# Kernel tuning notes

Hardware: AMD Instinct MI355X
Metric: run time of the kernel (lower is better)

Reference implementation:

```python
import jax, jax.numpy as jnp
import numpy as np

N, A, C = 65536, 512, 1000


def setup_inputs() -> dict:
    key = jax.random.key(0)
    k1, k2, k3, k4, k5 = jax.random.split(key, 5)
    return {
        "features": jax.random.normal(k1, (N, A), dtype=jnp.float32),
        "labels": jax.random.randint(k2, (N,), 0, C),
        "count": jax.random.uniform(k3, (C,), dtype=jnp.float32) * 100.0,
        "mean": jax.random.normal(k4, (C, A), dtype=jnp.float32),
        "cov": jax.random.uniform(k5, (C, A), dtype=jnp.float32),
    }


def reference(features, labels, count, mean, cov):
    # Per-class counts and feature sums via segment reduction (math identical to
    # the torch onehot-expand NxCxA construction, but O(N*A) instead of O(N*C*A)).
    c = count.shape[0]
    ones = jnp.ones((features.shape[0],), dtype=features.dtype)
    n_c = jax.ops.segment_sum(ones, labels, num_segments=c)            # [C]
    sums = jax.ops.segment_sum(features, labels, num_segments=c)      # [C, A]
    amt = jnp.where(n_c == 0, 1.0, n_c)                                # Amount_CxA (zeros -> 1)
    ave = sums / amt[:, None]                                          # ave_CxA
    diff = features - ave[labels]                                      # onehot*(x - ave) per row
    var = jax.ops.segment_sum(diff * diff, labels, num_segments=c) / amt[:, None]
    # EMA blend weight; torch sets NaN (0/0) entries to 0.
    denom = n_c + count
    w = jnp.where(denom == 0, 0.0, n_c / jnp.where(denom == 0, 1.0, denom))[:, None]  # [C,1]
    cov_new = cov * (1.0 - w) + var * w + w * (1.0 - w) * (mean - ave) ** 2
    mean_new = mean * (1.0 - w) + ave * w
    count_new = count + n_c
    return cov_new, mean_new, count_new
```

## Files before the change

### kernel.cpp

```cpp
#include <hip/hip_runtime.h>

constexpr int N_ROWS  = 65536;
constexpr int N_FEAT  = 512;
constexpr int N_FEAT2 = N_FEAT / 2;
constexpr int N_CLS   = 1000;


__global__ __launch_bounds__(1024) void hist_scan_kernel(
    const int* __restrict__ labels, int* __restrict__ offs, int* __restrict__ cursor)
{
    __shared__ int bins[1024];
    __shared__ int tmp[1024];
    const int t = threadIdx.x;
    bins[t] = 0;
    __syncthreads();

    const int4* __restrict__ l4 = (const int4*)labels;
    #pragma unroll 4
    for (int i = t; i < N_ROWS / 4; i += 1024) {
        int4 v = l4[i];
        atomicAdd(&bins[v.x], 1); atomicAdd(&bins[v.y], 1);
        atomicAdd(&bins[v.z], 1); atomicAdd(&bins[v.w], 1);
    }
    __syncthreads();

    const int v = bins[t];
    tmp[t] = v;
    __syncthreads();
    for (int d = 1; d < 1024; d <<= 1) {
        int x = (t >= d) ? tmp[t - d] : 0;
        __syncthreads();
        tmp[t] += x;
        __syncthreads();
    }
    const int excl = tmp[t] - v;
    offs[t] = excl;
    cursor[t] = excl;
    if (t == 0) offs[1024] = N_ROWS;
}

__global__ __launch_bounds__(256) void scatter_kernel(
    const int* __restrict__ labels, int* __restrict__ cursor, int* __restrict__ perm)
{
    const int i = blockIdx.x * blockDim.x + threadIdx.x;
    const int4 v = ((const int4*)labels)[i];
    const int r = i * 4;
    perm[atomicAdd(&cursor[v.x], 1)] = r + 0;
    perm[atomicAdd(&cursor[v.y], 1)] = r + 1;
    perm[atomicAdd(&cursor[v.z], 1)] = r + 2;
    perm[atomicAdd(&cursor[v.w], 1)] = r + 3;
}

__global__ __launch_bounds__(256) void estimator_main(
    const float* __restrict__ features,
    const float* __restrict__ count,
    const float* __restrict__ mean,
    const float* __restrict__ cov,
    const int* __restrict__ offs,
    const int* __restrict__ perm,
    float* __restrict__ out)
{
    const int c = blockIdx.x;
    const int t = threadIdx.x;
    const int start = offs[c];
    const int n = offs[c + 1] - start;

    __shared__ int sh[256];
    const float2* __restrict__ f2 = (const float2*)features;

    float sx = 0.f, sy = 0.f, qx = 0.f, qy = 0.f;

    for (int base = 0; base < n; base += 256) {
        const int chunk = min(256, n - base);
        __syncthreads();
        if (t < chunk) sh[t] = perm[start + base + t];
        __syncthreads();
        int j = 0;
        for (; j + 8 <= chunk; j += 8) {
            const int r0 = sh[j+0], r1 = sh[j+1], r2 = sh[j+2], r3 = sh[j+3];
            const int r4 = sh[j+4], r5 = sh[j+5], r6 = sh[j+6], r7 = sh[j+7];
            const float2 v0 = f2[(size_t)r0 * N_FEAT2 + t];
            const float2 v1 = f2[(size_t)r1 * N_FEAT2 + t];
            const float2 v2 = f2[(size_t)r2 * N_FEAT2 + t];
            const float2 v3 = f2[(size_t)r3 * N_FEAT2 + t];
            const float2 v4 = f2[(size_t)r4 * N_FEAT2 + t];
            const float2 v5 = f2[(size_t)r5 * N_FEAT2 + t];
            const float2 v6 = f2[(size_t)r6 * N_FEAT2 + t];
            const float2 v7 = f2[(size_t)r7 * N_FEAT2 + t];
            sx += v0.x; sy += v0.y; qx += v0.x*v0.x; qy += v0.y*v0.y;
            sx += v1.x; sy += v1.y; qx += v1.x*v1.x; qy += v1.y*v1.y;
            sx += v2.x; sy += v2.y; qx += v2.x*v2.x; qy += v2.y*v2.y;
            sx += v3.x; sy += v3.y; qx += v3.x*v3.x; qy += v3.y*v3.y;
            sx += v4.x; sy += v4.y; qx += v4.x*v4.x; qy += v4.y*v4.y;
            sx += v5.x; sy += v5.y; qx += v5.x*v5.x; qy += v5.y*v5.y;
            sx += v6.x; sy += v6.y; qx += v6.x*v6.x; qy += v6.y*v6.y;
            sx += v7.x; sy += v7.y; qx += v7.x*v7.x; qy += v7.y*v7.y;
        }
        for (; j < chunk; ++j) {
            const float2 v = f2[(size_t)sh[j] * N_FEAT2 + t];
            sx += v.x; sy += v.y; qx += v.x*v.x; qy += v.y*v.y;
        }
    }

    const float fn  = (float)n;
    const float amt = (n > 0) ? fn : 1.0f;
    const float inv = 1.0f / amt;
    const float avx = sx * inv, avy = sy * inv;
    const float vrx = qx * inv - avx * avx;
    const float vry = qy * inv - avy * avy;

    const float cnt   = count[c];
    const float denom = fn + cnt;
    const float w     = (denom == 0.f) ? 0.f : fn / denom;
    const float omw   = 1.0f - w;

    const float2 mv = ((const float2*)mean)[c * N_FEAT2 + t];
    const float2 cv = ((const float2*)cov)[c * N_FEAT2 + t];
    const float dx = mv.x - avx, dy = mv.y - avy;

    float2 covn, meann;
    covn.x  = cv.x * omw + vrx * w + w * omw * dx * dx;
    covn.y  = cv.y * omw + vry * w + w * omw * dy * dy;
    meann.x = mv.x * omw + avx * w;
    meann.y = mv.y * omw + avy * w;

    ((float2*)out)[c * N_FEAT2 + t] = covn;
    ((float2*)(out + N_CLS * N_FEAT))[c * N_FEAT2 + t] = meann;
    if (t == 0) out[2 * N_CLS * N_FEAT + c] = cnt + fn;
}

extern "C" void kernel_launch(void* const* d_in, const int* in_sizes, int n_in,
                              void* d_out, int out_size, void* d_ws, size_t ws_size,
                              hipStream_t stream) {
    const float* features = (const float*)d_in[0];
    const int*   labels   = (const int*)d_in[1];
    const float* count    = (const float*)d_in[2];
    const float* mean     = (const float*)d_in[3];
    const float* cov      = (const float*)d_in[4];
    float* out = (float*)d_out;

    char* ws = (char*)d_ws;
    int* offs   = (int*)(ws + 0);
    int* cursor = (int*)(ws + 8192);
    int* perm   = (int*)(ws + 12288);

    hist_scan_kernel<<<1, 1024, 0, stream>>>(labels, offs, cursor);
    scatter_kernel<<<N_ROWS / 4 / 256, 256, 0, stream>>>(labels, cursor, perm);
    estimator_main<<<N_CLS, 256, 0, stream>>>(features, count, mean, cov,
                                              offs, perm, out);
}
```

Baseline: 233.6 us.

## Parallelize label histogram across blocks and use float4 two-row gathers in estimator

```diff
diff --git a/kernel.cpp b/kernel.cpp
--- a/kernel.cpp
+++ b/kernel.cpp
@@ -2,29 +2,33 @@
 
 constexpr int N_ROWS  = 65536;
 constexpr int N_FEAT  = 512;
-constexpr int N_FEAT2 = N_FEAT / 2;
+constexpr int N_FEAT4 = N_FEAT / 4;
 constexpr int N_CLS   = 1000;
 
 
-__global__ __launch_bounds__(1024) void hist_scan_kernel(
-    const int* __restrict__ labels, int* __restrict__ offs, int* __restrict__ cursor)
+__global__ __launch_bounds__(256) void hist_kernel(
+    const int* __restrict__ labels, int* __restrict__ bins)
 {
-    __shared__ int bins[1024];
+    __shared__ int lbins[1024];
+    const int t = threadIdx.x;
+    lbins[t] = 0; lbins[t+256] = 0; lbins[t+512] = 0; lbins[t+768] = 0;
+    __syncthreads();
+    const int4 v = ((const int4*)labels)[blockIdx.x * 256 + t];
+    atomicAdd(&lbins[v.x], 1); atomicAdd(&lbins[v.y], 1);
+    atomicAdd(&lbins[v.z], 1); atomicAdd(&lbins[v.w], 1);
+    __syncthreads();
+    for (int i = t; i < N_CLS; i += 256) {
+        int c = lbins[i];
+        if (c) atomicAdd(&bins[i], c);
+    }
+}
+
+__global__ __launch_bounds__(1024) void scan_kernel(
+    const int* __restrict__ bins, int* __restrict__ offs, int* __restrict__ cursor)
+{
     __shared__ int tmp[1024];
     const int t = threadIdx.x;
-    bins[t] = 0;
-    __syncthreads();
-
-    const int4* __restrict__ l4 = (const int4*)labels;
-    #pragma unroll 4
-    for (int i = t; i < N_ROWS / 4; i += 1024) {
-        int4 v = l4[i];
-        atomicAdd(&bins[v.x], 1); atomicAdd(&bins[v.y], 1);
-        atomicAdd(&bins[v.z], 1); atomicAdd(&bins[v.w], 1);
-    }
-    __syncthreads();
-
-    const int v = bins[t];
+    const int v = (t < N_CLS) ? bins[t] : 0;
     tmp[t] = v;
     __syncthreads();
     for (int d = 1; d < 1024; d <<= 1) {
@@ -62,13 +66,19 @@
 {
     const int c = blockIdx.x;
     const int t = threadIdx.x;
+    const int half = t >> 7;
+    const int col  = t & 127;
     const int start = offs[c];
     const int n = offs[c + 1] - start;
 
     __shared__ int sh[256];
-    const float2* __restrict__ f2 = (const float2*)features;
+    __shared__ float4 red_s[128];
+    __shared__ float4 red_q[128];
 
-    float sx = 0.f, sy = 0.f, qx = 0.f, qy = 0.f;
+    const float4* __restrict__ f4 = (const float4*)features;
+
+    float s0 = 0.f, s1 = 0.f, s2 = 0.f, s3 = 0.f;
+    float q0 = 0.f, q1 = 0.f, q2 = 0.f, q3 = 0.f;
 
     for (int base = 0; base < n; base += 256) {
         const int chunk = min(256, n - base);
@@ -76,57 +86,86 @@
         if (t < chunk) sh[t] = perm[start + base + t];
         __syncthreads();
         int j = 0;
-        for (; j + 8 <= chunk; j += 8) {
-            const int r0 = sh[j+0], r1 = sh[j+1], r2 = sh[j+2], r3 = sh[j+3];
-            const int r4 = sh[j+4], r5 = sh[j+5], r6 = sh[j+6], r7 = sh[j+7];
-            const float2 v0 = f2[(size_t)r0 * N_FEAT2 + t];
-            const float2 v1 = f2[(size_t)r1 * N_FEAT2 + t];
-            const float2 v2 = f2[(size_t)r2 * N_FEAT2 + t];
-            const float2 v3 = f2[(size_t)r3 * N_FEAT2 + t];
-            const float2 v4 = f2[(size_t)r4 * N_FEAT2 + t];
-            const float2 v5 = f2[(size_t)r5 * N_FEAT2 + t];
-            const float2 v6 = f2[(size_t)r6 * N_FEAT2 + t];
-            const float2 v7 = f2[(size_t)r7 * N_FEAT2 + t];
-            sx += v0.x; sy += v0.y; qx += v0.x*v0.x; qy += v0.y*v0.y;
-            sx += v1.x; sy += v1.y; qx += v1.x*v1.x; qy += v1.y*v1.y;
-            sx += v2.x; sy += v2.y; qx += v2.x*v2.x; qy += v2.y*v2.y;
-            sx += v3.x; sy += v3.y; qx += v3.x*v3.x; qy += v3.y*v3.y;
-            sx += v4.x; sy += v4.y; qx += v4.x*v4.x; qy += v4.y*v4.y;
-            sx += v5.x; sy += v5.y; qx += v5.x*v5.x; qy += v5.y*v5.y;
-            sx += v6.x; sy += v6.y; qx += v6.x*v6.x; qy += v6.y*v6.y;
-            sx += v7.x; sy += v7.y; qx += v7.x*v7.x; qy += v7.y*v7.y;
+        for (; j + 16 <= chunk; j += 16) {
+            const int r0 = sh[j +  0 + half], r1 = sh[j +  2 + half];
+            const int r2 = sh[j +  4 + half], r3 = sh[j +  6 + half];
+            const int r4 = sh[j +  8 + half], r5 = sh[j + 10 + half];
+            const int r6 = sh[j + 12 + half], r7 = sh[j + 14 + half];
+            const float4 v0 = f4[(size_t)r0 * N_FEAT4 + col];
+            const float4 v1 = f4[(size_t)r1 * N_FEAT4 + col];
+            const float4 v2 = f4[(size_t)r2 * N_FEAT4 + col];
+            const float4 v3 = f4[(size_t)r3 * N_FEAT4 + col];
+            const float4 v4 = f4[(size_t)r4 * N_FEAT4 + col];
+            const float4 v5 = f4[(size_t)r5 * N_FEAT4 + col];
+            const float4 v6 = f4[(size_t)r6 * N_FEAT4 + col];
+            const float4 v7 = f4[(size_t)r7 * N_FEAT4 + col];
+            #define ACC(v) \
+                s0 += v.x; q0 = fmaf(v.x, v.x, q0); \
+                s1 += v.y; q1 = fmaf(v.y, v.y, q1); \
+                s2 += v.z; q2 = fmaf(v.z, v.z, q2); \
+                s3 += v.w; q3 = fmaf(v.w, v.w, q3);
+            ACC(v0) ACC(v1) ACC(v2) ACC(v3) ACC(v4) ACC(v5) ACC(v6) ACC(v7)
+            #undef ACC
         }
-        for (; j < chunk; ++j) {
-            const float2 v = f2[(size_t)sh[j] * N_FEAT2 + t];
-            sx += v.x; sy += v.y; qx += v.x*v.x; qy += v.y*v.y;
+        if (j < chunk) {
+            #pragma unroll
+            for (int u = 0; u < 8; ++u) {
+                const int idx = j + 2 * u + half;
+                const int r = (idx < chunk) ? sh[idx] : sh[j];
+                const float w = (idx < chunk) ? 1.f : 0.f;
+                const float4 v = f4[(size_t)r * N_FEAT4 + col];
+                const float vx = v.x * w, vy = v.y * w, vz = v.z * w, vw = v.w * w;
+                s0 += vx; q0 = fmaf(vx, v.x, q0);
+                s1 += vy; q1 = fmaf(vy, v.y, q1);
+                s2 += vz; q2 = fmaf(vz, v.z, q2);
+                s3 += vw; q3 = fmaf(vw, v.w, q3);
+            }
         }
     }
 
-    const float fn  = (float)n;
-    const float amt = (n > 0) ? fn : 1.0f;
-    const float inv = 1.0f / amt;
-    const float avx = sx * inv, avy = sy * inv;
-    const float vrx = qx * inv - avx * avx;
-    const float vry = qy * inv - avy * avy;
+    __syncthreads();
+    if (half == 1) {
+        red_s[col] = make_float4(s0, s1, s2, s3);
+        red_q[col] = make_float4(q0, q1, q2, q3);
+    }
+    __syncthreads();
+    if (half == 0) {
+        const float4 rs = red_s[col], rq = red_q[col];
+        s0 += rs.x; s1 += rs.y; s2 += rs.z; s3 += rs.w;
+        q0 += rq.x; q1 += rq.y; q2 += rq.z; q3 += rq.w;
 
-    const float cnt   = count[c];
-    const float denom = fn + cnt;
-    const float w     = (denom == 0.f) ? 0.f : fn / denom;
-    const float omw   = 1.0f - w;
+        const float fn  = (float)n;
+        const float amt = (n > 0) ? fn : 1.0f;
+        const float inv = 1.0f / amt;
+        const float a0 = s0 * inv, a1 = s1 * inv, a2 = s2 * inv, a3 = s3 * inv;
+        const float vr0 = q0 * inv - a0 * a0;
+        const float vr1 = q1 * inv - a1 * a1;
+        const float vr2 = q2 * inv - a2 * a2;
+        const float vr3 = q3 * inv - a3 * a3;
 
-    const float2 mv = ((const float2*)mean)[c * N_FEAT2 + t];
-    const float2 cv = ((const float2*)cov)[c * N_FEAT2 + t];
-    const float dx = mv.x - avx, dy = mv.y - avy;
+        const float cnt   = count[c];
+        const float denom = fn + cnt;
+        const float w     = (denom == 0.f) ? 0.f : fn / denom;
+        const float omw   = 1.0f - w;
 
-    float2 covn, meann;
-    covn.x  = cv.x * omw + vrx * w + w * omw * dx * dx;
-    covn.y  = cv.y * omw + vry * w + w * omw * dy * dy;
-    meann.x = mv.x * omw + avx * w;
-    meann.y = mv.y * omw + avy * w;
+        const float4 mv = ((const float4*)mean)[c * N_FEAT4 + col];
+        const float4 cv = ((const float4*)cov)[c * N_FEAT4 + col];
+        const float d0 = mv.x - a0, d1 = mv.y - a1, d2 = mv.z - a2, d3 = mv.w - a3;
 
-    ((float2*)out)[c * N_FEAT2 + t] = covn;
-    ((float2*)(out + N_CLS * N_FEAT))[c * N_FEAT2 + t] = meann;
-    if (t == 0) out[2 * N_CLS * N_FEAT + c] = cnt + fn;
+        float4 covn, meann;
+        covn.x  = cv.x * omw + vr0 * w + w * omw * d0 * d0;
+        covn.y  = cv.y * omw + vr1 * w + w * omw * d1 * d1;
+        covn.z  = cv.z * omw + vr2 * w + w * omw * d2 * d2;
+        covn.w  = cv.w * omw + vr3 * w + w * omw * d3 * d3;
+        meann.x = mv.x * omw + a0 * w;
+        meann.y = mv.y * omw + a1 * w;
+        meann.z = mv.z * omw + a2 * w;
+        meann.w = mv.w * omw + a3 * w;
+
+        ((float4*)out)[c * N_FEAT4 + col] = covn;
+        ((float4*)(out + N_CLS * N_FEAT))[c * N_FEAT4 + col] = meann;
+        if (t == 0) out[2 * N_CLS * N_FEAT + c] = cnt + fn;
+    }
 }
 
 extern "C" void kernel_launch(void* const* d_in, const int* in_sizes, int n_in,
@@ -140,11 +179,14 @@
     float* out = (float*)d_out;
 
     char* ws = (char*)d_ws;
-    int* offs   = (int*)(ws + 0);
-    int* cursor = (int*)(ws + 8192);
-    int* perm   = (int*)(ws + 12288);
+    int* bins   = (int*)(ws + 0);
+    int* offs   = (int*)(ws + 4096);
+    int* cursor = (int*)(ws + 12288);
+    int* perm   = (int*)(ws + 16384);
 
-    hist_scan_kernel<<<1, 1024, 0, stream>>>(labels, offs, cursor);
+    hipMemsetAsync(bins, 0, 1024 * sizeof(int), stream);
+    hist_kernel<<<N_ROWS / 4 / 256, 256, 0, stream>>>(labels, bins);
+    scan_kernel<<<1, 1024, 0, stream>>>(bins, offs, cursor);
     scatter_kernel<<<N_ROWS / 4 / 256, 256, 0, stream>>>(labels, cursor, perm);
     estimator_main<<<N_CLS, 256, 0, stream>>>(features, count, mean, cov,
                                               offs, perm, out);
```

Result: faster. 226.8 us (-2.9%).
